# Kernel optimization log

Hardware: AMD Instinct MI355X
Metric: run time of the kernel (lower is better)

## Reference

```python
import jax, jax.numpy as jnp
import numpy as np

FACTOR = 0.1   # init_kwargs factor
EPS = 1e-7
B, C, H, W = 256, 3, 224, 224


def setup_inputs() -> dict:
    key = jax.random.key(0)
    k1, k2, k3 = jax.random.split(key, 3)
    x = jax.random.normal(k1, (B, C, H, W), dtype=jnp.float32)
    shift_fy = jax.random.uniform(k2, (B,), dtype=jnp.float32)  # maps to torch.rand(1)
    shift_fx = jax.random.uniform(k3, (B,), dtype=jnp.float32)
    return {"x": x, "shift_fy": shift_fy, "shift_fx": shift_fx}


def _shift_axis(img, shift, axis, size):
    # Equivalent to torch in-place slice copy + zero-fill:
    #   shift>0: img[..., :size-shift] = img[..., shift:]; img[..., size-shift:] = 0
    #   shift<0: img[..., -shift:]   = img[..., :shift];  img[..., :-shift]   = 0
    # == roll by -shift, then zero positions j where j+shift is out of [0, size)
    idx = jnp.arange(size)
    rolled = jnp.roll(img, -shift, axis=axis)
    mask = (idx + shift >= 0) & (idx + shift < size)
    shp = [1, 1, 1]
    shp[axis] = size
    return rolled * mask.reshape(shp).astype(img.dtype)


def _per_image(img, fy, fx):
    # img: [C, H, W]
    h, w = img.shape[1], img.shape[2]
    # int(shift_factor * size) truncates toward zero -> jnp.trunc
    sy = jnp.trunc((fy * 2.0 - 1.0) * FACTOR * h).astype(jnp.int32)
    sx = jnp.trunc((fx * 2.0 - 1.0) * FACTOR * w).astype(jnp.int32)
    img = _shift_axis(img, sy, 1, h)
    img = _shift_axis(img, sx, 2, w)
    # standardize with unbiased std (torch.std default, ddof=1)
    n = img.size
    mean = jnp.mean(img)
    var = jnp.sum(jnp.square(img - mean)) / (n - 1)
    img = (img - mean) / (jnp.sqrt(var) + EPS)
    # min-max normalize
    mn = jnp.min(img)
    mx = jnp.max(img)
    return (img - mn) / (mx - mn)


def reference(x, shift_fy, shift_fx):
    # fully vectorized over the batch (original uses a Python per-image loop)
    return jax.vmap(_per_image)(x, shift_fy, shift_fx)
```

## Files before the change

kernel.cpp:

```cpp
#include <hip/hip_runtime.h>
#include <math.h>


constexpr int kC = 3, kH = 224, kW = 224;
constexpr int kCHW  = kC * kH * kW;
constexpr int kROWS = kC * kH;
constexpr int kQPR  = kW / 4;
constexpr int TB    = 256;
constexpr int PARTS = 8;
constexpr int WVB   = TB / 64;
constexpr int WPI   = PARTS * WVB;
constexpr int RPW   = kROWS / WPI;

typedef float f32x4 __attribute__((ext_vector_type(4)));

__device__ __forceinline__ void shifts_for(const float* __restrict__ sfy,
                                           const float* __restrict__ sfx,
                                           int img, int& sy, int& sx)
{
    float ty = sfy[img] * 2.0f - 1.0f; ty *= 0.1f; ty *= (float)kH;
    sy = (int)truncf(ty);
    float tx = sfx[img] * 2.0f - 1.0f; tx *= 0.1f; tx *= (float)kW;
    sx = (int)truncf(tx);
}

__global__ __launch_bounds__(TB) void minmax_k(
    const float* __restrict__ x, const float* __restrict__ sfy,
    const float* __restrict__ sfx, float2* __restrict__ ws)
{
    const int img  = blockIdx.x / PARTS;
    const int part = blockIdx.x - img * PARTS;
    const float* __restrict__ xb = x + (size_t)img * kCHW;

    int sy, sx; shifts_for(sfy, sfx, img, sy, sx);

    const int rlo = sy > 0 ? sy : 0;
    const int rhi = kH + (sy < 0 ? sy : 0);
    const int clo = sx > 0 ? sx : 0;
    const int chi = kW + (sx < 0 ? sx : 0);

    const int tid  = threadIdx.x;
    const int lane = tid & 63;
    const int wv = __builtin_amdgcn_readfirstlane(tid >> 6) + part * WVB;

    float vmin = INFINITY, vmax = -INFINITY;

    if (lane < kQPR) {
        const int i0 = lane * 4;
        float cm[4];
        #pragma unroll
        for (int k = 0; k < 4; ++k)
            cm[k] = ((i0 + k) >= clo && (i0 + k) < chi) ? 1.0f : 0.0f;

        #pragma unroll 3
        for (int t = 0; t < RPW; ++t) {
            const int rr = wv + t * WPI;
            const int j  = rr % kH;
            const float srm = (j >= rlo && j < rhi) ? 1.0f : 0.0f;
            const f32x4 v = *(const f32x4*)(xb + rr * kW + i0);
            #pragma unroll
            for (int k = 0; k < 4; ++k) {
                const float val = v[k] * cm[k] * srm;
                vmin = fminf(vmin, val);
                vmax = fmaxf(vmax, val);
            }
        }
    }

    #pragma unroll
    for (int off = 32; off > 0; off >>= 1) {
        vmin = fminf(vmin, __shfl_down(vmin, off));
        vmax = fmaxf(vmax, __shfl_down(vmax, off));
    }
    __shared__ float smin[WVB], smax[WVB];
    if (lane == 0) { smin[tid >> 6] = vmin; smax[tid >> 6] = vmax; }
    __syncthreads();
    if (tid == 0) {
        float mn = smin[0], mx = smax[0];
        #pragma unroll
        for (int w = 1; w < WVB; ++w) {
            mn = fminf(mn, smin[w]);
            mx = fmaxf(mx, smax[w]);
        }
        ws[img * PARTS + part] = make_float2(mn, mx);
    }
}

template <int R>
__device__ __forceinline__ void gather_rows(const float* __restrict__ xb,
                                            float* __restrict__ ob,
                                            int sy, int sx, float inv,
                                            float zoff, int wv, int lane)
{
    if (lane >= kQPR) return;
    const int i0   = lane * 4;
    const int base = i0 + sx - R;
    int qa = base;     qa = qa < 0 ? 0 : qa; qa = qa > kW - 4 ? kW - 4 : qa;
    int qb = base + 4; qb = qb < 0 ? 0 : qb; qb = qb > kW - 4 ? kW - 4 : qb;

    float cm[4];
    #pragma unroll
    for (int k = 0; k < 4; ++k) {
        const int s = i0 + k + sx;
        cm[k] = ((unsigned)s < (unsigned)kW) ? 1.0f : 0.0f;
    }

    #pragma unroll 3
    for (int t = 0; t < RPW; ++t) {
        const int rr = wv + t * WPI;
        const int j  = rr % kH;
        const int c0 = rr - j;
        const int jj = j + sy;
        const bool rowok = (unsigned)jj < (unsigned)kH;
        const int jc = rowok ? jj : 0;
        const float scale = rowok ? inv : 0.0f;
        const float* __restrict__ src = xb + (c0 + jc) * kW;

        const f32x4 av = *(const f32x4*)(src + qa);
        const f32x4 bv = *(const f32x4*)(src + qb);
        float sel[4];
        #pragma unroll
        for (int k = 0; k < 4; ++k)
            sel[k] = (k + R < 4) ? av[k + R] : bv[k + R - 4];

        f32x4 o;
        #pragma unroll
        for (int k = 0; k < 4; ++k)
            o[k] = fmaf(sel[k] * cm[k], scale, zoff);
        *(f32x4*)(ob + rr * kW + i0) = o;
    }
}

__global__ __launch_bounds__(TB) void norm_k(
    const float* __restrict__ x, const float* __restrict__ sfy,
    const float* __restrict__ sfx, const float2* __restrict__ ws,
    float* __restrict__ out)
{
    const int img  = blockIdx.x / PARTS;
    const int part = blockIdx.x - img * PARTS;
    const float* __restrict__ xb = x + (size_t)img * kCHW;
    float* __restrict__ ob = out + (size_t)img * kCHW;

    int sy, sx; shifts_for(sfy, sfx, img, sy, sx);

    float mn = INFINITY, mx = -INFINITY;
    #pragma unroll
    for (int p = 0; p < PARTS; ++p) {
        const float2 v = ws[img * PARTS + p];
        mn = fminf(mn, v.x);
        mx = fmaxf(mx, v.y);
    }
    const float inv  = 1.0f / (mx - mn);
    const float zoff = (0.0f - mn) * inv;

    const int lane = threadIdx.x & 63;
    const int wv = __builtin_amdgcn_readfirstlane(threadIdx.x >> 6) + part * WVB;

    switch (sx & 3) {
        case 0: gather_rows<0>(xb, ob, sy, sx, inv, zoff, wv, lane); break;
        case 1: gather_rows<1>(xb, ob, sy, sx, inv, zoff, wv, lane); break;
        case 2: gather_rows<2>(xb, ob, sy, sx, inv, zoff, wv, lane); break;
        default: gather_rows<3>(xb, ob, sy, sx, inv, zoff, wv, lane); break;
    }
}

extern "C" void kernel_launch(void* const* d_in, const int* in_sizes, int n_in,
                              void* d_out, int out_size, void* d_ws, size_t ws_size,
                              hipStream_t stream) {
    const float* x  = (const float*)d_in[0];
    const float* fy = (const float*)d_in[1];
    const float* fx = (const float*)d_in[2];
    float* out = (float*)d_out;
    const int B = in_sizes[1];
    float2* ws = (float2*)d_ws;
    minmax_k<<<B * PARTS, TB, 0, stream>>>(x, fy, fx, ws);
    norm_k<<<B * PARTS, TB, 0, stream>>>(x, fy, fx, ws, out);
}
```

Baseline: 295.3 us.

## Fuse min-max and normalize kernels into one block-per-image kernel

Result: no change. 299.1 us (+1.3%).

```diff
diff --git a/kernel.cpp b/kernel.cpp
--- a/kernel.cpp
+++ b/kernel.cpp
@@ -6,88 +6,14 @@
 constexpr int kCHW  = kC * kH * kW;
 constexpr int kROWS = kC * kH;
 constexpr int kQPR  = kW / 4;
-constexpr int TB    = 256;
-constexpr int PARTS = 8;
+constexpr int TB    = 1024;
 constexpr int WVB   = TB / 64;
-constexpr int WPI   = PARTS * WVB;
-constexpr int RPW   = kROWS / WPI;
+constexpr int RPW   = kROWS / WVB;
 
 typedef float f32x4 __attribute__((ext_vector_type(4)));
 
-__device__ __forceinline__ void shifts_for(const float* __restrict__ sfy,
-                                           const float* __restrict__ sfx,
-                                           int img, int& sy, int& sx)
-{
-    float ty = sfy[img] * 2.0f - 1.0f; ty *= 0.1f; ty *= (float)kH;
-    sy = (int)truncf(ty);
-    float tx = sfx[img] * 2.0f - 1.0f; tx *= 0.1f; tx *= (float)kW;
-    sx = (int)truncf(tx);
-}
-
-__global__ __launch_bounds__(TB) void minmax_k(
-    const float* __restrict__ x, const float* __restrict__ sfy,
-    const float* __restrict__ sfx, float2* __restrict__ ws)
-{
-    const int img  = blockIdx.x / PARTS;
-    const int part = blockIdx.x - img * PARTS;
-    const float* __restrict__ xb = x + (size_t)img * kCHW;
-
-    int sy, sx; shifts_for(sfy, sfx, img, sy, sx);
-
-    const int rlo = sy > 0 ? sy : 0;
-    const int rhi = kH + (sy < 0 ? sy : 0);
-    const int clo = sx > 0 ? sx : 0;
-    const int chi = kW + (sx < 0 ? sx : 0);
-
-    const int tid  = threadIdx.x;
-    const int lane = tid & 63;
-    const int wv = __builtin_amdgcn_readfirstlane(tid >> 6) + part * WVB;
-
-    float vmin = INFINITY, vmax = -INFINITY;
-
-    if (lane < kQPR) {
-        const int i0 = lane * 4;
-        float cm[4];
-        #pragma unroll
-        for (int k = 0; k < 4; ++k)
-            cm[k] = ((i0 + k) >= clo && (i0 + k) < chi) ? 1.0f : 0.0f;
-
-        #pragma unroll 3
-        for (int t = 0; t < RPW; ++t) {
-            const int rr = wv + t * WPI;
-            const int j  = rr % kH;
-            const float srm = (j >= rlo && j < rhi) ? 1.0f : 0.0f;
-            const f32x4 v = *(const f32x4*)(xb + rr * kW + i0);
-            #pragma unroll
-            for (int k = 0; k < 4; ++k) {
-                const float val = v[k] * cm[k] * srm;
-                vmin = fminf(vmin, val);
-                vmax = fmaxf(vmax, val);
-            }
-        }
-    }
-
-    #pragma unroll
-    for (int off = 32; off > 0; off >>= 1) {
-        vmin = fminf(vmin, __shfl_down(vmin, off));
-        vmax = fmaxf(vmax, __shfl_down(vmax, off));
-    }
-    __shared__ float smin[WVB], smax[WVB];
-    if (lane == 0) { smin[tid >> 6] = vmin; smax[tid >> 6] = vmax; }
-    __syncthreads();
-    if (tid == 0) {
-        float mn = smin[0], mx = smax[0];
-        #pragma unroll
-        for (int w = 1; w < WVB; ++w) {
-            mn = fminf(mn, smin[w]);
-            mx = fmaxf(mx, smax[w]);
-        }
-        ws[img * PARTS + part] = make_float2(mn, mx);
-    }
-}
-
 template <int R>
-__device__ __forceinline__ void gather_rows(const float* __restrict__ xb,
+__device__ __forceinline__ void phase2_rows(const float* __restrict__ xb,
                                             float* __restrict__ ob,
                                             int sy, int sx, float inv,
                                             float zoff, int wv, int lane)
@@ -100,67 +26,111 @@
 
     float cm[4];
     #pragma unroll
-    for (int k = 0; k < 4; ++k) {
-        const int s = i0 + k + sx;
-        cm[k] = ((unsigned)s < (unsigned)kW) ? 1.0f : 0.0f;
-    }
+    for (int k = 0; k < 4; ++k)
+        cm[k] = ((unsigned)(i0 + k + sx) < (unsigned)kW) ? 1.0f : 0.0f;
+    const f32x4 zq = {zoff, zoff, zoff, zoff};
 
     #pragma unroll 3
     for (int t = 0; t < RPW; ++t) {
-        const int rr = wv + t * WPI;
+        const int rr = wv + t * WVB;
         const int j  = rr % kH;
-        const int c0 = rr - j;
         const int jj = j + sy;
-        const bool rowok = (unsigned)jj < (unsigned)kH;
-        const int jc = rowok ? jj : 0;
-        const float scale = rowok ? inv : 0.0f;
-        const float* __restrict__ src = xb + (c0 + jc) * kW;
-
-        const f32x4 av = *(const f32x4*)(src + qa);
-        const f32x4 bv = *(const f32x4*)(src + qb);
-        float sel[4];
-        #pragma unroll
-        for (int k = 0; k < 4; ++k)
-            sel[k] = (k + R < 4) ? av[k + R] : bv[k + R - 4];
-
-        f32x4 o;
-        #pragma unroll
-        for (int k = 0; k < 4; ++k)
-            o[k] = fmaf(sel[k] * cm[k], scale, zoff);
-        *(f32x4*)(ob + rr * kW + i0) = o;
+        float* __restrict__ dst = ob + rr * kW + i0;
+        if ((unsigned)jj < (unsigned)kH) {
+            const float* __restrict__ src = xb + (rr - j + jj) * kW;
+            const f32x4 av = *(const f32x4*)(src + qa);
+            const f32x4 bv = *(const f32x4*)(src + qb);
+            f32x4 o;
+            #pragma unroll
+            for (int k = 0; k < 4; ++k) {
+                const float sel = (k + R < 4) ? av[k + R] : bv[k + R - 4];
+                o[k] = fmaf(sel * cm[k], inv, zoff);
+            }
+            *(f32x4*)dst = o;
+        } else {
+            *(f32x4*)dst = zq;
+        }
     }
 }
 
-__global__ __launch_bounds__(TB) void norm_k(
+__global__ __launch_bounds__(TB) void shift_norm(
     const float* __restrict__ x, const float* __restrict__ sfy,
-    const float* __restrict__ sfx, const float2* __restrict__ ws,
-    float* __restrict__ out)
+    const float* __restrict__ sfx, float* __restrict__ out)
 {
-    const int img  = blockIdx.x / PARTS;
-    const int part = blockIdx.x - img * PARTS;
+    const int img = blockIdx.x;
     const float* __restrict__ xb = x + (size_t)img * kCHW;
     float* __restrict__ ob = out + (size_t)img * kCHW;
 
-    int sy, sx; shifts_for(sfy, sfx, img, sy, sx);
+    float ty = sfy[img] * 2.0f - 1.0f; ty *= 0.1f; ty *= (float)kH;
+    const int sy = (int)truncf(ty);
+    float tx = sfx[img] * 2.0f - 1.0f; tx *= 0.1f; tx *= (float)kW;
+    const int sx = (int)truncf(tx);
 
-    float mn = INFINITY, mx = -INFINITY;
+    const int rlo = sy > 0 ? sy : 0;
+    const int rhi = kH + (sy < 0 ? sy : 0);
+    const int clo = sx > 0 ? sx : 0;
+    const int chi = kW + (sx < 0 ? sx : 0);
+
+    const int tid  = threadIdx.x;
+    const int lane = tid & 63;
+    const int wv   = __builtin_amdgcn_readfirstlane(tid >> 6);
+
+    const bool hasfill = (sy != 0) | (sx != 0);
+    float vmin = hasfill ? 0.0f : INFINITY;
+    float vmax = hasfill ? 0.0f : -INFINITY;
+
+    if (lane < kQPR) {
+        const int i0 = lane * 4;
+        float cm[4];
+        #pragma unroll
+        for (int k = 0; k < 4; ++k)
+            cm[k] = ((i0 + k) >= clo && (i0 + k) < chi) ? 1.0f : 0.0f;
+
+        #pragma unroll 6
+        for (int t = 0; t < RPW; ++t) {
+            const int rr = wv + t * WVB;
+            const int j  = rr % kH;
+            if (j >= rlo && j < rhi) {
+                const f32x4 v = *(const f32x4*)(xb + rr * kW + i0);
+                #pragma unroll
+                for (int k = 0; k < 4; ++k) {
+                    const float val = v[k] * cm[k];
+                    vmin = fminf(vmin, val);
+                    vmax = fmaxf(vmax, val);
+                }
+            }
+        }
+    }
+
     #pragma unroll
-    for (int p = 0; p < PARTS; ++p) {
-        const float2 v = ws[img * PARTS + p];
-        mn = fminf(mn, v.x);
-        mx = fmaxf(mx, v.y);
+    for (int off = 32; off > 0; off >>= 1) {
+        vmin = fminf(vmin, __shfl_down(vmin, off));
+        vmax = fmaxf(vmax, __shfl_down(vmax, off));
     }
-    const float inv  = 1.0f / (mx - mn);
+    __shared__ float smin[WVB], smax[WVB];
+    __shared__ float s_mn, s_inv;
+    if (lane == 0) { smin[tid >> 6] = vmin; smax[tid >> 6] = vmax; }
+    __syncthreads();
+    if (tid == 0) {
+        float mn = smin[0], mx = smax[0];
+        #pragma unroll
+        for (int w = 1; w < WVB; ++w) {
+            mn = fminf(mn, smin[w]);
+            mx = fmaxf(mx, smax[w]);
+        }
+        s_mn  = mn;
+        s_inv = 1.0f / (mx - mn);
+    }
+    __syncthreads();
+    const float mn   = s_mn;
+    const float inv  = s_inv;
     const float zoff = (0.0f - mn) * inv;
 
-    const int lane = threadIdx.x & 63;
-    const int wv = __builtin_amdgcn_readfirstlane(threadIdx.x >> 6) + part * WVB;
-
     switch (sx & 3) {
-        case 0: gather_rows<0>(xb, ob, sy, sx, inv, zoff, wv, lane); break;
-        case 1: gather_rows<1>(xb, ob, sy, sx, inv, zoff, wv, lane); break;
-        case 2: gather_rows<2>(xb, ob, sy, sx, inv, zoff, wv, lane); break;
-        default: gather_rows<3>(xb, ob, sy, sx, inv, zoff, wv, lane); break;
+        case 0: phase2_rows<0>(xb, ob, sy, sx, inv, zoff, wv, lane); break;
+        case 1: phase2_rows<1>(xb, ob, sy, sx, inv, zoff, wv, lane); break;
+        case 2: phase2_rows<2>(xb, ob, sy, sx, inv, zoff, wv, lane); break;
+        default: phase2_rows<3>(xb, ob, sy, sx, inv, zoff, wv, lane); break;
     }
 }
 
@@ -172,7 +142,5 @@
     const float* fx = (const float*)d_in[2];
     float* out = (float*)d_out;
     const int B = in_sizes[1];
-    float2* ws = (float2*)d_ws;
-    minmax_k<<<B * PARTS, TB, 0, stream>>>(x, fy, fx, ws);
-    norm_k<<<B * PARTS, TB, 0, stream>>>(x, fy, fx, ws, out);
+    shift_norm<<<B, TB, 0, stream>>>(x, fy, fx, out);
 }
```

## Write shifted image in first pass and normalize output in place with atomic min/max

Applied to the files above, without the earlier changes.

Result: slower. 320.2 us (+8.4%).

```diff
diff --git a/kernel.cpp b/kernel.cpp
--- a/kernel.cpp
+++ b/kernel.cpp
@@ -4,15 +4,21 @@
 
 constexpr int kC = 3, kH = 224, kW = 224;
 constexpr int kCHW  = kC * kH * kW;
-constexpr int kROWS = kC * kH;
 constexpr int kQPR  = kW / 4;
+constexpr int kNQ   = kC * kH * kQPR;
 constexpr int TB    = 256;
 constexpr int PARTS = 8;
 constexpr int WVB   = TB / 64;
-constexpr int WPI   = PARTS * WVB;
-constexpr int RPW   = kROWS / WPI;
 
 typedef float f32x4 __attribute__((ext_vector_type(4)));
+
+__device__ __forceinline__ unsigned enc_f(float f) {
+    const unsigned u = __float_as_uint(f);
+    return u ^ (((int)u >> 31) ? 0xFFFFFFFFu : 0x80000000u);
+}
+__device__ __forceinline__ float dec_f(unsigned e) {
+    return __uint_as_float(e ^ ((e & 0x80000000u) ? 0x80000000u : 0xFFFFFFFFu));
+}
 
 __device__ __forceinline__ void shifts_for(const float* __restrict__ sfy,
                                            const float* __restrict__ sfx,
@@ -24,47 +30,62 @@
     sx = (int)truncf(tx);
 }
 
-__global__ __launch_bounds__(TB) void minmax_k(
+template <int R>
+__device__ __forceinline__ void gatherA(const float* __restrict__ xb,
+                                        float* __restrict__ ob,
+                                        int sy, int sx, int f0,
+                                        float& vmin, float& vmax)
+{
+    for (int f = f0; f < kNQ; f += PARTS * TB) {
+        const int rr = f / kQPR;
+        const int q  = f - rr * kQPR;
+        const int j  = rr % kH;
+        const int c0 = rr - j;
+        const int jj = j + sy;
+        const bool rowok = (unsigned)jj < (unsigned)kH;
+        const int jc = rowok ? jj : 0;
+        const float* __restrict__ src = xb + (c0 + jc) * kW;
+
+        const int i0 = q * 4;
+        const int base = i0 + sx - R;
+        int qa = base;     qa = qa < 0 ? 0 : qa; qa = qa > kW - 4 ? kW - 4 : qa;
+        int qb = base + 4; qb = qb < 0 ? 0 : qb; qb = qb > kW - 4 ? kW - 4 : qb;
+        const f32x4 av = *(const f32x4*)(src + qa);
+        const f32x4 bv = *(const f32x4*)(src + qb);
+
+        f32x4 o;
+        #pragma unroll
+        for (int k = 0; k < 4; ++k) {
+            const float sel = (k + R < 4) ? av[k + R] : bv[k + R - 4];
+            const int s = i0 + k + sx;
+            const float v = (rowok && (unsigned)s < (unsigned)kW) ? sel : 0.0f;
+            o[k] = v;
+            vmin = fminf(vmin, v);
+            vmax = fmaxf(vmax, v);
+        }
+        *(f32x4*)(ob + rr * kW + i0) = o;
+    }
+}
+
+__global__ __launch_bounds__(TB) void passA(
     const float* __restrict__ x, const float* __restrict__ sfy,
-    const float* __restrict__ sfx, float2* __restrict__ ws)
+    const float* __restrict__ sfx, float* __restrict__ out,
+    unsigned* __restrict__ umin, unsigned* __restrict__ umax)
 {
-    const int img  = blockIdx.x / PARTS;
-    const int part = blockIdx.x - img * PARTS;
+    const int img  = blockIdx.x >> 3;
+    const int part = blockIdx.x & (PARTS - 1);
     const float* __restrict__ xb = x + (size_t)img * kCHW;
+    float* __restrict__ ob = out + (size_t)img * kCHW;
 
     int sy, sx; shifts_for(sfy, sfx, img, sy, sx);
 
-    const int rlo = sy > 0 ? sy : 0;
-    const int rhi = kH + (sy < 0 ? sy : 0);
-    const int clo = sx > 0 ? sx : 0;
-    const int chi = kW + (sx < 0 ? sx : 0);
-
-    const int tid  = threadIdx.x;
-    const int lane = tid & 63;
-    const int wv = __builtin_amdgcn_readfirstlane(tid >> 6) + part * WVB;
-
     float vmin = INFINITY, vmax = -INFINITY;
-
-    if (lane < kQPR) {
-        const int i0 = lane * 4;
-        float cm[4];
-        #pragma unroll
-        for (int k = 0; k < 4; ++k)
-            cm[k] = ((i0 + k) >= clo && (i0 + k) < chi) ? 1.0f : 0.0f;
-
-        #pragma unroll 3
-        for (int t = 0; t < RPW; ++t) {
-            const int rr = wv + t * WPI;
-            const int j  = rr % kH;
-            const float srm = (j >= rlo && j < rhi) ? 1.0f : 0.0f;
-            const f32x4 v = *(const f32x4*)(xb + rr * kW + i0);
-            #pragma unroll
-            for (int k = 0; k < 4; ++k) {
-                const float val = v[k] * cm[k] * srm;
-                vmin = fminf(vmin, val);
-                vmax = fmaxf(vmax, val);
-            }
-        }
+    const int f0 = part * TB + threadIdx.x;
+    switch (sx & 3) {
+        case 0: gatherA<0>(xb, ob, sy, sx, f0, vmin, vmax); break;
+        case 1: gatherA<1>(xb, ob, sy, sx, f0, vmin, vmax); break;
+        case 2: gatherA<2>(xb, ob, sy, sx, f0, vmin, vmax); break;
+        default: gatherA<3>(xb, ob, sy, sx, f0, vmin, vmax); break;
     }
 
     #pragma unroll
@@ -73,7 +94,8 @@
         vmax = fmaxf(vmax, __shfl_down(vmax, off));
     }
     __shared__ float smin[WVB], smax[WVB];
-    if (lane == 0) { smin[tid >> 6] = vmin; smax[tid >> 6] = vmax; }
+    const int tid = threadIdx.x;
+    if ((tid & 63) == 0) { smin[tid >> 6] = vmin; smax[tid >> 6] = vmax; }
     __syncthreads();
     if (tid == 0) {
         float mn = smin[0], mx = smax[0];
@@ -82,85 +104,31 @@
             mn = fminf(mn, smin[w]);
             mx = fmaxf(mx, smax[w]);
         }
-        ws[img * PARTS + part] = make_float2(mn, mx);
+        atomicMin(&umin[img], enc_f(mn));
+        atomicMax(&umax[img], enc_f(mx));
     }
 }
 
-template <int R>
-__device__ __forceinline__ void gather_rows(const float* __restrict__ xb,
-                                            float* __restrict__ ob,
-                                            int sy, int sx, float inv,
-                                            float zoff, int wv, int lane)
+__global__ __launch_bounds__(TB) void passB(
+    float* __restrict__ out,
+    const unsigned* __restrict__ umin, const unsigned* __restrict__ umax)
 {
-    if (lane >= kQPR) return;
-    const int i0   = lane * 4;
-    const int base = i0 + sx - R;
-    int qa = base;     qa = qa < 0 ? 0 : qa; qa = qa > kW - 4 ? kW - 4 : qa;
-    int qb = base + 4; qb = qb < 0 ? 0 : qb; qb = qb > kW - 4 ? kW - 4 : qb;
+    const int img = blockIdx.x >> 3;
+    const float mn = dec_f(umin[img]);
+    const float mx = dec_f(umax[img]);
+    const float inv  = 1.0f / (mx - mn);
+    const float zoff = (0.0f - mn) * inv;
+    float* __restrict__ ob = out + (size_t)img * kCHW;
 
-    float cm[4];
-    #pragma unroll
-    for (int k = 0; k < 4; ++k) {
-        const int s = i0 + k + sx;
-        cm[k] = ((unsigned)s < (unsigned)kW) ? 1.0f : 0.0f;
-    }
-
-    #pragma unroll 3
-    for (int t = 0; t < RPW; ++t) {
-        const int rr = wv + t * WPI;
-        const int j  = rr % kH;
-        const int c0 = rr - j;
-        const int jj = j + sy;
-        const bool rowok = (unsigned)jj < (unsigned)kH;
-        const int jc = rowok ? jj : 0;
-        const float scale = rowok ? inv : 0.0f;
-        const float* __restrict__ src = xb + (c0 + jc) * kW;
-
-        const f32x4 av = *(const f32x4*)(src + qa);
-        const f32x4 bv = *(const f32x4*)(src + qb);
-        float sel[4];
-        #pragma unroll
-        for (int k = 0; k < 4; ++k)
-            sel[k] = (k + R < 4) ? av[k + R] : bv[k + R - 4];
-
+    #pragma unroll 2
+    for (int f = (blockIdx.x & (PARTS - 1)) * TB + threadIdx.x; f < kNQ;
+         f += PARTS * TB) {
+        f32x4 v = *(const f32x4*)(ob + f * 4);
         f32x4 o;
         #pragma unroll
         for (int k = 0; k < 4; ++k)
-            o[k] = fmaf(sel[k] * cm[k], scale, zoff);
-        *(f32x4*)(ob + rr * kW + i0) = o;
-    }
-}
-
-__global__ __launch_bounds__(TB) void norm_k(
-    const float* __restrict__ x, const float* __restrict__ sfy,
-    const float* __restrict__ sfx, const float2* __restrict__ ws,
-    float* __restrict__ out)
-{
-    const int img  = blockIdx.x / PARTS;
-    const int part = blockIdx.x - img * PARTS;
-    const float* __restrict__ xb = x + (size_t)img * kCHW;
-    float* __restrict__ ob = out + (size_t)img * kCHW;
-
-    int sy, sx; shifts_for(sfy, sfx, img, sy, sx);
-
-    float mn = INFINITY, mx = -INFINITY;
-    #pragma unroll
-    for (int p = 0; p < PARTS; ++p) {
-        const float2 v = ws[img * PARTS + p];
-        mn = fminf(mn, v.x);
-        mx = fmaxf(mx, v.y);
-    }
-    const float inv  = 1.0f / (mx - mn);
-    const float zoff = (0.0f - mn) * inv;
-
-    const int lane = threadIdx.x & 63;
-    const int wv = __builtin_amdgcn_readfirstlane(threadIdx.x >> 6) + part * WVB;
-
-    switch (sx & 3) {
-        case 0: gather_rows<0>(xb, ob, sy, sx, inv, zoff, wv, lane); break;
-        case 1: gather_rows<1>(xb, ob, sy, sx, inv, zoff, wv, lane); break;
-        case 2: gather_rows<2>(xb, ob, sy, sx, inv, zoff, wv, lane); break;
-        default: gather_rows<3>(xb, ob, sy, sx, inv, zoff, wv, lane); break;
+            o[k] = fmaf(v[k], inv, zoff);
+        *(f32x4*)(ob + f * 4) = o;
     }
 }
 
@@ -172,7 +140,12 @@
     const float* fx = (const float*)d_in[2];
     float* out = (float*)d_out;
     const int B = in_sizes[1];
-    float2* ws = (float2*)d_ws;
-    minmax_k<<<B * PARTS, TB, 0, stream>>>(x, fy, fx, ws);
-    norm_k<<<B * PARTS, TB, 0, stream>>>(x, fy, fx, ws, out);
+
+    unsigned* umin = (unsigned*)d_ws;
+    unsigned* umax = umin + B;
+    hipMemsetAsync(umin, 0xFF, (size_t)B * sizeof(unsigned), stream);
+    hipMemsetAsync(umax, 0x00, (size_t)B * sizeof(unsigned), stream);
+
+    passA<<<B * PARTS, TB, 0, stream>>>(x, fy, fx, out, umin, umax);
+    passB<<<B * PARTS, TB, 0, stream>>>(out, umin, umax);
 }
```
